# Optimization experiments

Measured on AMD Instinct MI355X. Metric: run time of the kernel, lower is better.

Reference implementation:

```python
import jax, jax.numpy as jnp
import numpy as np

D_MODEL = 2048
NUM_HEADS = 32
HEAD_DIM = D_MODEL // NUM_HEADS  # 64
ROPE_BASE = 10000.0


def _rope_cos_sin(seq_len, head_dim, dtype):
    inv_freq = 1.0 / (ROPE_BASE ** (jnp.arange(0, head_dim, 2, dtype=jnp.float32) / head_dim))
    freqs = jnp.arange(seq_len, dtype=jnp.float32)[:, None] * inv_freq[None, :]  # (S, Dh/2)
    emb = jnp.concatenate([freqs, freqs], axis=-1)  # (S, Dh)
    return emb.astype(dtype), jnp.cos(emb).astype(dtype), jnp.sin(emb).astype(dtype)


def _rotate_half(x):
    x1, x2 = jnp.split(x, 2, axis=-1)
    return jnp.concatenate([-x2, x1], axis=-1)


def setup_inputs() -> dict:
    key = jax.random.key(0)
    k1, k2, k3, k4 = jax.random.split(key, 4)
    B, S, D = 1, 2048, D_MODEL
    x = jax.random.normal(k1, (B, S, D), dtype=jnp.float32)
    Wqkv = jax.random.normal(k2, (3 * D, D), dtype=jnp.float32) * 0.02
    Wo = jax.random.normal(k3, (D, D), dtype=jnp.float32) * 0.02
    gate = jax.random.normal(k4, (D,), dtype=jnp.float32) * 0.1
    return {"x": x, "Wqkv": Wqkv, "Wo": Wo, "gate": gate}


def reference(x, Wqkv, Wo, gate):
    B, S, D = x.shape
    H, Dh = NUM_HEADS, HEAD_DIM
    residual = x

    # fused QKV projection (torch Linear: y = x @ W.T)
    qkv = jnp.einsum('bsd,ed->bse', x, Wqkv).reshape(B, S, 3, H, Dh)
    q, k, v = qkv[:, :, 0], qkv[:, :, 1], qkv[:, :, 2]  # each (B, S, H, Dh)

    # RoPE
    _, cos, sin = _rope_cos_sin(S, Dh, x.dtype)
    cos = cos[None, :, None, :]  # (1, S, 1, Dh)
    sin = sin[None, :, None, :]
    q = q * cos + _rotate_half(q) * sin
    k = k * cos + _rotate_half(k) * sin

    # causal SDPA
    scale = 1.0 / np.sqrt(Dh)
    scores = jnp.einsum('bqhd,bkhd->bhqk', q, k) * scale  # (B, H, S, S)
    causal = jnp.tril(jnp.ones((S, S), dtype=bool))
    scores = jnp.where(causal[None, None], scores, jnp.finfo(scores.dtype).min)
    probs = jax.nn.softmax(scores, axis=-1)
    attn = jnp.einsum('bhqk,bkhd->bqhd', probs, v).reshape(B, S, D)

    out = jnp.einsum('bsd,ed->bse', attn, Wo)
    # HeoGate: learned per-channel gated residual (assumption; see notes)
    return residual + gate * out
```

## Files before the change

kernel.cpp:

```cpp
#include <hip/hip_runtime.h>
#include <hip/hip_bf16.h>
#include <cstdint>
#include <cstddef>

typedef __hip_bfloat16 bf16;
typedef short short8 __attribute__((ext_vector_type(8)));
typedef float f32x4 __attribute__((ext_vector_type(4)));

#define S_LEN 2048
#define DMODEL 2048
#define NQKV 6144
#define NHEADS 32
#define HDIM 64
#define ROPE_L2 0.4152410118609203f

__device__ __forceinline__ void async_copy16(const bf16* g, bf16* l) {
  __builtin_amdgcn_global_load_lds(
      (const __attribute__((address_space(1))) void*)g,
      (__attribute__((address_space(3))) void*)l, 16, 0, 0);
}

__device__ __forceinline__ f32x4 mfma_bf16(short8 a, short8 b, f32x4 c) {
  return __builtin_amdgcn_mfma_f32_16x16x32_bf16(a, b, c, 0, 0, 0);
}

__global__ __launch_bounds__(256) void cvt3_kernel(const float* __restrict__ sx,
                                                   bf16* __restrict__ dx,
                                                   const float* __restrict__ sw,
                                                   bf16* __restrict__ dw,
                                                   const float* __restrict__ so,
                                                   bf16* __restrict__ dov) {
  int i = blockIdx.x * 256 + threadIdx.x;
  const float* s;
  bf16* d;
  if (i < 1048576) {
    s = sx; d = dx;
  } else if (i < 4194304) {
    s = sw; d = dw; i -= 1048576;
  } else {
    s = so; d = dov; i -= 4194304;
  }
  const float4 v = ((const float4*)s)[i];
  union { bf16 h[4]; ushort4 u; } tmp;
  tmp.h[0] = __float2bfloat16(v.x);
  tmp.h[1] = __float2bfloat16(v.y);
  tmp.h[2] = __float2bfloat16(v.z);
  tmp.h[3] = __float2bfloat16(v.w);
  ((ushort4*)d)[i] = tmp.u;
}

__global__ __launch_bounds__(256) void gemm_qkv(const bf16* __restrict__ A,
                                                const bf16* __restrict__ W,
                                                bf16* __restrict__ q_ws,
                                                bf16* __restrict__ k_ws,
                                                bf16* __restrict__ v_ws) {
  constexpr int K = DMODEL;
  __shared__ bf16 smem[8192];
  const int tid = threadIdx.x;
  const int wave = tid >> 6, lane = tid & 63;
  const int wm = wave >> 1, wn = wave & 1;
  const int m0 = blockIdx.y * 128, n0 = blockIdx.x * 128;
  const int sr = wave * 16 + (lane >> 2);
  const int swc = (((lane & 3) ^ ((lane >> 3) & 3)) * 8);
  const int fr = lane & 15, fq = lane >> 4;
  const int rdc = ((fq ^ ((fr >> 1) & 3)) * 8);

  const f32x4 zero = {0.f, 0.f, 0.f, 0.f};
  f32x4 acc[4][4];
  for (int i = 0; i < 4; ++i)
    for (int j = 0; j < 4; ++j) acc[i][j] = zero;

  for (int kt = 0; kt < K; kt += 32) {
    __syncthreads();
    for (int i2 = 0; i2 < 2; ++i2) {
      async_copy16(A + (size_t)(m0 + i2 * 64 + sr) * K + kt + swc,
                   &smem[(i2 * 64 + wave * 16) * 32]);
      async_copy16(W + (size_t)(n0 + i2 * 64 + sr) * K + kt + swc,
                   &smem[4096 + (i2 * 64 + wave * 16) * 32]);
    }
    __syncthreads();
    short8 a[4], b[4];
    for (int i = 0; i < 4; ++i)
      a[i] = *(const short8*)&smem[(wm * 64 + i * 16 + fr) * 32 + rdc];
    for (int j = 0; j < 4; ++j)
      b[j] = *(const short8*)&smem[4096 + (wn * 64 + j * 16 + fr) * 32 + rdc];
    for (int i = 0; i < 4; ++i)
      for (int j = 0; j < 4; ++j)
        acc[i][j] = mfma_bf16(a[i], b[j], acc[i][j]);
  }

  const int colb = n0 + wn * 64;
  const int sect = colb >> 11;
  const int h = (colb & 2047) >> 6;
  const int col = fr, rq = fq * 4;

  if (sect < 2) {
    bf16* dst = ((sect == 0) ? q_ws : k_ws) + (size_t)h * S_LEN * HDIM;
    bf16* rep = smem + wave * 1152;
    const float f0 = exp2f(-(float)col * ROPE_L2);
    const float f1 = exp2f(-(float)(16 + col) * ROPE_L2);
    __syncthreads();
    for (int i = 0; i < 4; ++i) {
      const int base_s = m0 + wm * 64 + i * 16;
#pragma unroll
      for (int jl = 0; jl < 2; ++jl) {
        const int dh = jl * 16 + col;
        const float fr_ = (jl == 0) ? f0 : f1;
#pragma unroll
        for (int r = 0; r < 4; ++r) {
          const int srow = base_s + rq + r;
          float sn, cs;
          __sincosf((float)srow * fr_, &sn, &cs);
          const float xl = acc[i][jl][r], xh = acc[i][jl + 2][r];
          rep[(rq + r) * 72 + dh]      = __float2bfloat16(xl * cs - xh * sn);
          rep[(rq + r) * 72 + dh + 32] = __float2bfloat16(xh * cs + xl * sn);
        }
      }
#pragma unroll
      for (int p = 0; p < 2; ++p) {
        const int rr = p * 8 + (lane >> 3), ch = lane & 7;
        const uint4 vv = *(const uint4*)&rep[rr * 72 + ch * 8];
        *(uint4*)&dst[(size_t)(base_s + rr) * HDIM + ch * 8] = vv;
      }
    }
  } else {
    bf16* dst = v_ws + (size_t)h * HDIM * S_LEN;
    for (int j = 0; j < 4; ++j) {
      const int dh = j * 16 + col;
      for (int i = 0; i < 4; ++i) {
        const int s0 = m0 + wm * 64 + i * 16 + rq;
        union { bf16 hx[4]; uint2 u; } vk;
#pragma unroll
        for (int r = 0; r < 4; ++r) vk.hx[r] = __float2bfloat16(acc[i][j][r]);
        *(uint2*)&dst[(size_t)dh * S_LEN + s0] = vk.u;
      }
    }
  }
}

__global__ __launch_bounds__(256) void attn_kernel(const bf16* __restrict__ q_ws,
                                                   const bf16* __restrict__ k_ws,
                                                   const bf16* __restrict__ vt_ws,
                                                   bf16* __restrict__ attn_out) {
  const int bid = blockIdx.x;
  const int qt = 31 - (bid >> 5);
  const int h = bid & 31;

  const int tid = threadIdx.x, wave = tid >> 6, lane = tid & 63;
  const int col = lane & 15, fq = lane >> 4;
  const int q_glob = qt * 64 + wave * 16 + col;

  __shared__ bf16 Ks[2][64 * 64];
  __shared__ bf16 Vs[2][64 * 64];
  __shared__ bf16 Pl[4][16 * 72];
  bf16* pl = Pl[wave];

  const bf16* qh = q_ws + (size_t)h * S_LEN * HDIM;
  const bf16* kh = k_ws + (size_t)h * S_LEN * HDIM;
  const bf16* vh = vt_ws + (size_t)h * HDIM * S_LEN;

  const int srow = lane >> 3;
  const int slot = lane & 7;
  const int schunk = slot ^ srow;

  auto stage = [&](int kt, int buf) {
    const int k0 = kt * 64;
#pragma unroll
    for (int j = 0; j < 2; ++j) {
      const int r8 = (wave * 2 + j) * 8;
      async_copy16(kh + (size_t)(k0 + r8 + srow) * HDIM + schunk * 8,
                   &Ks[buf][r8 * 64]);
      async_copy16(vh + (size_t)(r8 + srow) * S_LEN + k0 + schunk * 8,
                   &Vs[buf][r8 * 64]);
    }
  };

  short8 qf[2];
#pragma unroll
  for (int ks = 0; ks < 2; ++ks)
    qf[ks] = *(const short8*)&qh[(size_t)q_glob * HDIM + ks * 32 + fq * 8];

  const f32x4 zero = {0.f, 0.f, 0.f, 0.f};
  f32x4 o_acc[4] = {zero, zero, zero, zero};
  float m_i = -1e30f, l_i = 0.f;

  stage(0, 0);

  for (int kt = 0; kt <= qt; ++kt) {
    const int buf = kt & 1;
    const int k0 = kt * 64;
    __syncthreads();
    if (kt < qt) stage(kt + 1, buf ^ 1);

    short8 kf[8];
#pragma unroll
    for (int n = 0; n < 4; ++n) {
      const int row = n * 16 + col;
#pragma unroll
      for (int ks = 0; ks < 2; ++ks)
        kf[n * 2 + ks] =
            *(const short8*)&Ks[buf][row * 64 + (((ks * 4 + fq) ^ (row & 7)) * 8)];
    }
    f32x4 s_acc[4] = {zero, zero, zero, zero};
#pragma unroll
    for (int n = 0; n < 4; ++n)
#pragma unroll
      for (int ks = 0; ks < 2; ++ks)
        s_acc[n] = mfma_bf16(kf[n * 2 + ks], qf[ks], s_acc[n]);

    short8 vf[8];
#pragma unroll
    for (int n = 0; n < 4; ++n) {
      const int row = n * 16 + col;
#pragma unroll
      for (int ks = 0; ks < 2; ++ks)
        vf[n * 2 + ks] =
            *(const short8*)&Vs[buf][row * 64 + (((ks * 4 + fq) ^ (row & 7)) * 8)];
    }

    if (kt == qt) {
#pragma unroll
      for (int n = 0; n < 4; ++n)
#pragma unroll
        for (int r = 0; r < 4; ++r)
          if (k0 + n * 16 + fq * 4 + r > q_glob) s_acc[n][r] = -1e30f;
    }

    float vmax = -1e30f;
#pragma unroll
    for (int n = 0; n < 4; ++n)
#pragma unroll
      for (int r = 0; r < 4; ++r) vmax = fmaxf(vmax, s_acc[n][r]);
    vmax = fmaxf(vmax, __shfl_xor(vmax, 16, 64));
    vmax = fmaxf(vmax, __shfl_xor(vmax, 32, 64));
    const float mnew = fmaxf(m_i, vmax);
    const float alpha = __expf((m_i - mnew) * 0.125f);
    m_i = mnew;

    float rs = 0.f;
#pragma unroll
    for (int n = 0; n < 4; ++n)
#pragma unroll
      for (int r = 0; r < 4; ++r) {
        const float p = __expf((s_acc[n][r] - mnew) * 0.125f);
        s_acc[n][r] = p;
        rs += p;
      }
    rs += __shfl_xor(rs, 16, 64);
    rs += __shfl_xor(rs, 32, 64);
    l_i = l_i * alpha + rs;

#pragma unroll
    for (int n = 0; n < 4; ++n)
#pragma unroll
      for (int r = 0; r < 4; ++r) o_acc[n][r] *= alpha;

#pragma unroll
    for (int n = 0; n < 4; ++n) {
      union { bf16 hx[4]; uint2 u; } pk;
#pragma unroll
      for (int r = 0; r < 4; ++r) pk.hx[r] = __float2bfloat16(s_acc[n][r]);
      *(uint2*)&pl[col * 72 + n * 16 + fq * 4] = pk.u;
    }
    short8 pa[2];
#pragma unroll
    for (int ks = 0; ks < 2; ++ks)
      pa[ks] = *(const short8*)&pl[col * 72 + ks * 32 + fq * 8];

#pragma unroll
    for (int n = 0; n < 4; ++n)
#pragma unroll
      for (int ks = 0; ks < 2; ++ks)
        o_acc[n] = mfma_bf16(vf[n * 2 + ks], pa[ks], o_acc[n]);
  }

  const float inv = 1.0f / l_i;
#pragma unroll
  for (int n = 0; n < 4; ++n) {
#pragma unroll
    for (int r = 0; r < 4; ++r) o_acc[n][r] *= inv;
    union { bf16 hx[4]; uint2 u; } ok;
#pragma unroll
    for (int r = 0; r < 4; ++r) ok.hx[r] = __float2bfloat16(o_acc[n][r]);
    *(uint2*)&attn_out[(size_t)q_glob * DMODEL + h * HDIM + n * 16 + fq * 4] = ok.u;
  }
}

__global__ __launch_bounds__(256) void gemm_out(const bf16* __restrict__ A,
                                                const bf16* __restrict__ W,
                                                const float* __restrict__ xres,
                                                const float* __restrict__ gate,
                                                float* __restrict__ out) {
  constexpr int K = DMODEL;
  __shared__ bf16 As[64 * 32];
  __shared__ bf16 Bs[128 * 32];
  const int tid = threadIdx.x;
  const int wave = tid >> 6, lane = tid & 63;
  const int m0 = blockIdx.y * 64, n0 = blockIdx.x * 128;
  const int sr = lane >> 2;
  const int swc = (((lane & 3) ^ ((lane >> 3) & 3)) * 8);
  const int fr = lane & 15, fq = lane >> 4;
  const int rdc = ((fq ^ ((fr >> 1) & 3)) * 8);

  const f32x4 zero = {0.f, 0.f, 0.f, 0.f};
  f32x4 acc[4][2];
  for (int i = 0; i < 4; ++i)
    for (int j = 0; j < 2; ++j) acc[i][j] = zero;

  for (int kt = 0; kt < K; kt += 32) {
    __syncthreads();
    async_copy16(A + (size_t)(m0 + wave * 16 + sr) * K + kt + swc,
                 &As[(wave * 16) * 32]);
#pragma unroll
    for (int j = 0; j < 2; ++j)
      async_copy16(W + (size_t)(n0 + wave * 32 + j * 16 + sr) * K + kt + swc,
                   &Bs[(wave * 32 + j * 16) * 32]);
    __syncthreads();
    short8 a[4], b[2];
    for (int i = 0; i < 4; ++i)
      a[i] = *(const short8*)&As[(i * 16 + fr) * 32 + rdc];
    for (int j = 0; j < 2; ++j)
      b[j] = *(const short8*)&Bs[(wave * 32 + j * 16 + fr) * 32 + rdc];
    for (int i = 0; i < 4; ++i)
      for (int j = 0; j < 2; ++j)
        acc[i][j] = mfma_bf16(a[i], b[j], acc[i][j]);
  }

  const int col = fr, rq = fq * 4;
  for (int j = 0; j < 2; ++j) {
    const int cc = n0 + wave * 32 + j * 16 + col;
    const float g = gate[cc];
    for (int i = 0; i < 4; ++i) {
      const int base_row = m0 + i * 16 + rq;
      for (int r = 0; r < 4; ++r) {
        const size_t idx = (size_t)(base_row + r) * DMODEL + cc;
        out[idx] = xres[idx] + g * acc[i][j][r];
      }
    }
  }
}

extern "C" void kernel_launch(void* const* d_in, const int* in_sizes, int n_in,
                              void* d_out, int out_size, void* d_ws, size_t ws_size,
                              hipStream_t stream) {
  const float* x    = (const float*)d_in[0];
  const float* Wqkv = (const float*)d_in[1];
  const float* Wo   = (const float*)d_in[2];
  const float* gate = (const float*)d_in[3];
  float* out = (float*)d_out;

  char* ws = (char*)d_ws;
  const size_t MB = 1024 * 1024;
  bf16* xb      = (bf16*)(ws);
  bf16* wqkvb   = (bf16*)(ws + 8 * MB);
  bf16* wob     = (bf16*)(ws + 32 * MB);
  bf16* q_ws    = (bf16*)(ws + 40 * MB);
  bf16* k_ws    = (bf16*)(ws + 48 * MB);
  bf16* v_ws    = (bf16*)(ws + 56 * MB);
  bf16* attn_ws = (bf16*)(ws);

  cvt3_kernel<<<dim3(20480), 256, 0, stream>>>(x, xb, Wqkv, wqkvb, Wo, wob);

  gemm_qkv<<<dim3(NQKV / 128, DMODEL / 128), 256, 0, stream>>>(xb, wqkvb, q_ws, k_ws, v_ws);
  attn_kernel<<<dim3(1024), 256, 0, stream>>>(q_ws, k_ws, v_ws, attn_ws);
  gemm_out<<<dim3(DMODEL / 128, DMODEL / 64), 256, 0, stream>>>(attn_ws, wob, x, gate, out);
}
```

Baseline: 257.4 us.

## Rewrite QKV GEMM with 256x256 tiles and double-buffered async LDS pipeline

Switches the QKV projection GEMM from 128x128 tiles with 256 threads and a fully synchronous per-k-step load to 256x256 tiles with 512 threads. Global-to-LDS async copies are staged one to two k-steps ahead in a double buffer, with explicit vmcnt waits, barriers and raised MFMA priority to overlap memory with compute. This raises data reuse per block and hides load latency, but uses 128KB of LDS and launches only 192 blocks, which may underfill the GPU.

Measured after the change: 253.1 us. About the same (-1.7%).

```diff
diff --git a/kernel.cpp b/kernel.cpp
--- a/kernel.cpp
+++ b/kernel.cpp
@@ -49,45 +49,106 @@
   ((ushort4*)d)[i] = tmp.u;
 }
 
-__global__ __launch_bounds__(256) void gemm_qkv(const bf16* __restrict__ A,
-                                                const bf16* __restrict__ W,
-                                                bf16* __restrict__ q_ws,
-                                                bf16* __restrict__ k_ws,
-                                                bf16* __restrict__ v_ws) {
-  constexpr int K = DMODEL;
-  __shared__ bf16 smem[8192];
+#define QKV_NT 32
+#define QBAR() do { __builtin_amdgcn_s_barrier(); __builtin_amdgcn_sched_barrier(0); } while (0)
+#define WAITV(n) asm volatile("s_waitcnt vmcnt(" #n ")" ::: "memory")
+#define LGKM0() do { asm volatile("s_waitcnt lgkmcnt(0)" ::: "memory"); \
+                     __builtin_amdgcn_sched_barrier(0); } while (0)
+
+__global__ __launch_bounds__(512, 2) void gemm_qkv(const bf16* __restrict__ A,
+                                                   const bf16* __restrict__ W,
+                                                   bf16* __restrict__ q_ws,
+                                                   bf16* __restrict__ k_ws,
+                                                   bf16* __restrict__ v_ws) {
+  __shared__ bf16 smem[65536];
   const int tid = threadIdx.x;
   const int wave = tid >> 6, lane = tid & 63;
-  const int wm = wave >> 1, wn = wave & 1;
-  const int m0 = blockIdx.y * 128, n0 = blockIdx.x * 128;
-  const int sr = wave * 16 + (lane >> 2);
+  const int wm = wave >> 2, wn = wave & 3;
+  const int m0 = blockIdx.y * 256, n0 = blockIdx.x * 256;
   const int swc = (((lane & 3) ^ ((lane >> 3) & 3)) * 8);
   const int fr = lane & 15, fq = lane >> 4;
   const int rdc = ((fq ^ ((fr >> 1) & 3)) * 8);
+  const int srg = wave * 16 + (lane >> 2);
+
+  auto stageA = [&](int t_, int kk_, int off_) {
+#pragma unroll
+    for (int rd = 0; rd < 2; ++rd)
+      async_copy16(A + (size_t)(m0 + rd * 128 + srg) * DMODEL + t_ * 64 + kk_ * 32 + swc,
+                   &smem[off_ + (rd * 128 + wave * 16) * 32]);
+  };
+  auto stageB = [&](int t_, int kk_, int off_) {
+#pragma unroll
+    for (int rd = 0; rd < 2; ++rd)
+      async_copy16(W + (size_t)(n0 + rd * 128 + srg) * DMODEL + t_ * 64 + kk_ * 32 + swc,
+                   &smem[off_ + (rd * 128 + wave * 16) * 32]);
+  };
 
   const f32x4 zero = {0.f, 0.f, 0.f, 0.f};
-  f32x4 acc[4][4];
-  for (int i = 0; i < 4; ++i)
+  f32x4 acc[8][4];
+#pragma unroll
+  for (int i = 0; i < 8; ++i)
+#pragma unroll
     for (int j = 0; j < 4; ++j) acc[i][j] = zero;
-
-  for (int kt = 0; kt < K; kt += 32) {
-    __syncthreads();
-    for (int i2 = 0; i2 < 2; ++i2) {
-      async_copy16(A + (size_t)(m0 + i2 * 64 + sr) * K + kt + swc,
-                   &smem[(i2 * 64 + wave * 16) * 32]);
-      async_copy16(W + (size_t)(n0 + i2 * 64 + sr) * K + kt + swc,
-                   &smem[4096 + (i2 * 64 + wave * 16) * 32]);
-    }
-    __syncthreads();
-    short8 a[4], b[4];
-    for (int i = 0; i < 4; ++i)
-      a[i] = *(const short8*)&smem[(wm * 64 + i * 16 + fr) * 32 + rdc];
-    for (int j = 0; j < 4; ++j)
-      b[j] = *(const short8*)&smem[4096 + (wn * 64 + j * 16 + fr) * 32 + rdc];
-    for (int i = 0; i < 4; ++i)
-      for (int j = 0; j < 4; ++j)
-        acc[i][j] = mfma_bf16(a[i], b[j], acc[i][j]);
-  }
+  short8 a[4], b[4];
+
+  stageA(0, 0, 0);
+  stageB(0, 0, 16384);
+  stageA(0, 1, 8192);
+  stageB(0, 1, 24576);
+  stageA(1, 0, 32768);
+  stageB(1, 0, 32768 + 16384);
+  WAITV(8);
+  QBAR();
+
+#define LOAD_A(KK, MB, BC)                                                        \
+  {                                                                               \
+    const bf16* sA_ = &smem[(BC) * 32768 + (KK) * 8192];                          \
+    _Pragma("unroll") for (int mi = 0; mi < 4; ++mi)                              \
+        a[mi] = *(const short8*)&sA_[(wm * 128 + (MB) + mi * 16 + fr) * 32 + rdc];\
+  }
+#define LOAD_B(KK, BC)                                                            \
+  {                                                                               \
+    const bf16* sB_ = &smem[(BC) * 32768 + 16384 + (KK) * 8192];                  \
+    _Pragma("unroll") for (int n = 0; n < 4; ++n)                                 \
+        b[n] = *(const short8*)&sB_[(wn * 64 + n * 16 + fr) * 32 + rdc];          \
+  }
+#define MFMA16(MB)                                                                \
+  __builtin_amdgcn_s_setprio(1);                                                  \
+  _Pragma("unroll") for (int mi = 0; mi < 4; ++mi)                                \
+      _Pragma("unroll") for (int n = 0; n < 4; ++n)                               \
+          acc[(MB) / 16 + mi][n] = mfma_bf16(a[mi], b[n], acc[(MB) / 16 + mi][n]);\
+  __builtin_amdgcn_s_setprio(0);
+
+#pragma unroll 2
+  for (int t = 0; t < QKV_NT; ++t) {
+    const int bc = t & 1, bn = bc ^ 1;
+    LOAD_A(0, 0, bc); LOAD_B(0, bc);
+    if (t + 1 < QKV_NT) stageA(t + 1, 1, bn * 32768 + 8192);
+    QBAR(); LGKM0();
+    MFMA16(0);
+    QBAR();
+    LOAD_A(0, 64, bc);
+    if (t + 1 < QKV_NT) stageB(t + 1, 1, bn * 32768 + 24576);
+    QBAR(); LGKM0();
+    MFMA16(64);
+    if (t < QKV_NT - 1) { WAITV(8); } else { WAITV(0); }
+    QBAR();
+    LOAD_A(1, 64, bc); LOAD_B(1, bc);
+    if (t + 2 < QKV_NT) stageA(t + 2, 0, bc * 32768);
+    QBAR(); LGKM0();
+    MFMA16(64);
+    QBAR();
+    LOAD_A(1, 0, bc);
+    if (t + 2 < QKV_NT) stageB(t + 2, 0, bc * 32768 + 16384);
+    QBAR(); LGKM0();
+    MFMA16(0);
+    if (t < QKV_NT - 2) { WAITV(8); }
+    else if (t == QKV_NT - 2) { WAITV(4); }
+    QBAR();
+  }
+#undef LOAD_A
+#undef LOAD_B
+#undef MFMA16
 
   const int colb = n0 + wn * 64;
   const int sect = colb >> 11;
@@ -100,8 +161,8 @@
     const float f0 = exp2f(-(float)col * ROPE_L2);
     const float f1 = exp2f(-(float)(16 + col) * ROPE_L2);
     __syncthreads();
-    for (int i = 0; i < 4; ++i) {
-      const int base_s = m0 + wm * 64 + i * 16;
+    for (int m = 0; m < 8; ++m) {
+      const int base_s = m0 + wm * 128 + m * 16;
 #pragma unroll
       for (int jl = 0; jl < 2; ++jl) {
         const int dh = jl * 16 + col;
@@ -111,7 +172,7 @@
           const int srow = base_s + rq + r;
           float sn, cs;
           __sincosf((float)srow * fr_, &sn, &cs);
-          const float xl = acc[i][jl][r], xh = acc[i][jl + 2][r];
+          const float xl = acc[m][jl][r], xh = acc[m][jl + 2][r];
           rep[(rq + r) * 72 + dh]      = __float2bfloat16(xl * cs - xh * sn);
           rep[(rq + r) * 72 + dh + 32] = __float2bfloat16(xh * cs + xl * sn);
         }
@@ -127,11 +188,11 @@
     bf16* dst = v_ws + (size_t)h * HDIM * S_LEN;
     for (int j = 0; j < 4; ++j) {
       const int dh = j * 16 + col;
-      for (int i = 0; i < 4; ++i) {
-        const int s0 = m0 + wm * 64 + i * 16 + rq;
+      for (int m = 0; m < 8; ++m) {
+        const int s0 = m0 + wm * 128 + m * 16 + rq;
         union { bf16 hx[4]; uint2 u; } vk;
 #pragma unroll
-        for (int r = 0; r < 4; ++r) vk.hx[r] = __float2bfloat16(acc[i][j][r]);
+        for (int r = 0; r < 4; ++r) vk.hx[r] = __float2bfloat16(acc[m][j][r]);
         *(uint2*)&dst[(size_t)dh * S_LEN + s0] = vk.u;
       }
     }
@@ -361,7 +422,7 @@
 
   cvt3_kernel<<<dim3(20480), 256, 0, stream>>>(x, xb, Wqkv, wqkvb, Wo, wob);
 
-  gemm_qkv<<<dim3(NQKV / 128, DMODEL / 128), 256, 0, stream>>>(xb, wqkvb, q_ws, k_ws, v_ws);
+  gemm_qkv<<<dim3(NQKV / 256, S_LEN / 256), 512, 0, stream>>>(xb, wqkvb, q_ws, k_ws, v_ws);
   attn_kernel<<<dim3(1024), 256, 0, stream>>>(q_ws, k_ws, v_ws, attn_ws);
   gemm_out<<<dim3(DMODEL / 128, DMODEL / 64), 256, 0, stream>>>(attn_ws, wob, x, gate, out);
 }
```
